# Performance work log

Hardware: AMD Instinct MI355X
Metric: run time of the kernel (lower is better)

## Reference

```python
import jax, jax.numpy as jnp
import numpy as np

B, T, D, H = 4, 2048, 1024, 16
Hd = D // H


def setup_inputs() -> dict:
    key = jax.random.key(0)
    ks = jax.random.split(key, 6)
    s = 1.0 / np.sqrt(D)
    return {
        "x": jax.random.normal(ks[0], (B, T, D), dtype=jnp.float32),
        "mask": jnp.zeros((B, T), dtype=bool),
        "Wq": jax.random.normal(ks[1], (D, D), dtype=jnp.float32) * s,
        "bq": jnp.zeros((D,), dtype=jnp.float32),
        "Wk": jax.random.normal(ks[2], (D, D), dtype=jnp.float32) * s,
        "bk": jnp.zeros((D,), dtype=jnp.float32),
        "Wv": jax.random.normal(ks[3], (D, D), dtype=jnp.float32) * s,
        "bv": jnp.zeros((D,), dtype=jnp.float32),
        "Wo": jax.random.normal(ks[4], (D, D), dtype=jnp.float32) * s,
        "bo": jnp.zeros((D,), dtype=jnp.float32),
    }


def reference(x, mask, Wq, bq, Wk, bk, Wv, bv, Wo, bo):
    b, t, d = x.shape
    # projections -> [B, T, H, Hd]
    Q = (x @ Wq + bq).reshape(b, t, H, Hd)
    K = (x @ Wk + bk).reshape(b, t, H, Hd)
    V = (x @ Wv + bv).reshape(b, t, H, Hd)
    scale = jnp.asarray(Hd, x.dtype) ** -0.5
    # full score matrix [B, H, Tq, Tk] (matches the naive torch impl)
    attn = jnp.einsum("bqhd,bkhd->bhqk", Q, K) * scale
    attn = jnp.where(mask[:, None, None, :], jnp.asarray(-1e9, attn.dtype), attn)
    attn = jax.nn.softmax(attn, axis=-1)
    out = jnp.einsum("bhqk,bkhd->bqhd", attn, V).reshape(b, t, d)
    return out @ Wo + bo
```

## Files before the change

kernel.cpp:

```cpp
#include <hip/hip_runtime.h>

using bf16 = __bf16;
typedef bf16 bf16x4 __attribute__((ext_vector_type(4)));
typedef bf16 bf16x8 __attribute__((ext_vector_type(8)));
typedef float f32x4 __attribute__((ext_vector_type(4)));
typedef float f32x8 __attribute__((ext_vector_type(8)));

#define MFMA16(a, b, c) __builtin_amdgcn_mfma_f32_16x16x32_bf16(a, b, c, 0, 0, 0)

constexpr int Bb = 4, Tt = 2048, Dd = 1024, Hh = 16, Hd = 64;
constexpr int Mrows = Bb * Tt;
constexpr float CEXP = 0.18033688011112042f;

__device__ __forceinline__ void gload_lds16(const bf16* g, bf16* lds_base) {
  __builtin_amdgcn_global_load_lds((const __attribute__((address_space(1))) void*)g,
                                   (__attribute__((address_space(3))) void*)lds_base,
                                   16, 0, 0);
}

__global__ void cast_f32_bf16_kernel(const float* __restrict__ in, bf16* __restrict__ out) {
  size_t i = ((size_t)blockIdx.x * 256 + threadIdx.x) * 8;
  f32x8 v = *(const f32x8*)(in + i);
  *(bf16x8*)(out + i) = __builtin_convertvector(v, bf16x8);
}

__global__ void transpose_cast_w4_kernel(const float* __restrict__ Wq, const float* __restrict__ Wk,
                                         const float* __restrict__ Wv, const float* __restrict__ Wo,
                                         bf16* __restrict__ Wt, bf16* __restrict__ Wot) {
  __shared__ alignas(16) float tile[64][68];
  const int tid = threadIdx.x;
  const int n0 = blockIdx.x * 64, k0 = blockIdx.y * 64, z = blockIdx.z;
  const float* W = (z == 0) ? Wq : (z == 1) ? Wk : (z == 2) ? Wv : Wo;
  bf16* dst = (z == 3) ? Wot : (Wt + (size_t)z * Dd * Dd);
  const float scale = (z == 0) ? CEXP : 1.0f;
#pragma unroll
  for (int it = 0; it < 4; ++it) {
    int chunk = tid + it * 256;
    int kr = chunk >> 4, c4 = chunk & 15;
    f32x4 v = *(const f32x4*)(W + (size_t)(k0 + kr) * Dd + n0 + c4 * 4);
    *(f32x4*)&tile[kr][c4 * 4] = v * scale;
  }
  __syncthreads();
#pragma unroll
  for (int it = 0; it < 2; ++it) {
    int chunk = tid + it * 256;
    int n = chunk & 63, k8 = chunk >> 6;
    bf16x8 o;
#pragma unroll
    for (int j = 0; j < 8; ++j) o[j] = (bf16)tile[k8 * 8 + j][n];
    *(bf16x8*)(dst + (size_t)(n0 + n) * Dd + k0 + k8 * 8) = o;
  }
}

__global__ void pack_bias_kernel(const float* __restrict__ bq, const float* __restrict__ bk,
                                 const float* __restrict__ bv, float* __restrict__ outb) {
  int i = blockIdx.x * 256 + threadIdx.x;
  float v = (i < 1024) ? bq[i] * CEXP : (i < 2048 ? bk[i - 1024] : bv[i - 2048]);
  outb[i] = v;
}

constexpr int QBM = 128, QBN = 256, QBK = 32, QNT = Dd / QBK;

#define VMW(n) asm volatile("s_waitcnt vmcnt(" #n ")" ::: "memory")

__global__ __launch_bounds__(512, 2)
void gemm_qkv_kernel(const bf16* __restrict__ A, const bf16* __restrict__ Bt,
                     const float* __restrict__ bias, bf16* __restrict__ QK,
                     bf16* __restrict__ Vt) {
  constexpr int KD = Dd;
  __shared__ alignas(16) bf16 As[3][QBM * QBK];
  __shared__ alignas(16) bf16 Bs[3][QBN * QBK];
  const int tid = threadIdx.x;
  const int lane = tid & 63, wave = tid >> 6;
  const int col = lane & 15, quad = lane >> 4;
  const int wr = wave >> 2, wc = wave & 3;
  const size_t m0 = (size_t)blockIdx.x * QBM, n0 = (size_t)blockIdx.y * QBN;

  const int u = (lane & 7) ^ (lane >> 3);
  const int srow = 2 * (lane >> 3) + (u >> 2);
  const int scol = (u & 3) * 8;
  const bf16* Abase = A + (m0 + srow) * (size_t)KD + scol;
  const bf16* Bbase = Bt + (n0 + srow) * (size_t)KD + scol;

  const int pswz = (((col & 1) << 2) | quad) ^ (col >> 1);
  const int afb = wr * 2048 + (col >> 1) * 64 + pswz * 8;
  const int bfb = wc * 2048 + (col >> 1) * 64 + pswz * 8;

  f32x4 acc[4][4];
#pragma unroll
  for (int i = 0; i < 4; ++i)
#pragma unroll
    for (int j = 0; j < 4; ++j)
#pragma unroll
      for (int r = 0; r < 4; ++r) acc[i][j][r] = 0.f;

#define QSTAGE(t, sl) do { \
    gload_lds16(Abase + (size_t)(t) * QBK + (size_t)(wave * 16) * KD, &As[sl][wave * 512]); \
    gload_lds16(Bbase + (size_t)(t) * QBK + (size_t)(2 * wave) * 16 * KD, &Bs[sl][(2 * wave) * 512]); \
    gload_lds16(Bbase + (size_t)(t) * QBK + (size_t)(2 * wave + 1) * 16 * KD, &Bs[sl][(2 * wave + 1) * 512]); \
  } while (0)

#define QKV_TILE(cur, DOSTAGE, VM) do { \
    bf16x8 af[4], bfv[4]; \
    _Pragma("unroll") for (int j = 0; j < 4; ++j) bfv[j] = *(const bf16x8*)&Bs[cur][bfb + j * 512]; \
    _Pragma("unroll") for (int i = 0; i < 4; ++i) af[i] = *(const bf16x8*)&As[cur][afb + i * 512]; \
    DOSTAGE; \
    asm volatile("s_waitcnt lgkmcnt(0)" ::: "memory"); \
    __builtin_amdgcn_s_setprio(1); \
    _Pragma("unroll") for (int i = 0; i < 4; ++i) \
      _Pragma("unroll") for (int j = 0; j < 4; ++j) acc[i][j] = MFMA16(af[i], bfv[j], acc[i][j]); \
    __builtin_amdgcn_s_setprio(0); \
    VM; \
    __builtin_amdgcn_s_barrier(); \
  } while (0)

  QSTAGE(0, 0);
  QSTAGE(1, 1);
  VMW(3);
  __builtin_amdgcn_s_barrier();

#pragma unroll 1
  for (int t = 0; t < QNT - 2; t += 3) {
    QKV_TILE(0, QSTAGE(t + 2, 2), VMW(3));
    QKV_TILE(1, QSTAGE(t + 3, 0), VMW(3));
    QKV_TILE(2, QSTAGE(t + 4, 1), VMW(3));
  }
  QKV_TILE(0, (void)0, VMW(0));
  QKV_TILE(1, (void)0, (void)0);

  if (n0 < 2048) {
#pragma unroll
    for (int i = 0; i < 4; ++i)
#pragma unroll
      for (int j = 0; j < 4; ++j) {
        size_t row = m0 + wr * 64 + i * 16 + quad * 4;
        size_t c = n0 + wc * 64 + j * 16 + col;
        float bv = bias[c];
#pragma unroll
        for (int r = 0; r < 4; ++r) QK[(row + r) * 2048 + c] = (bf16)(acc[i][j][r] + bv);
      }
  } else {
#pragma unroll
    for (int i = 0; i < 4; ++i)
#pragma unroll
      for (int j = 0; j < 4; ++j) {
        size_t row = m0 + wr * 64 + i * 16 + quad * 4;
        int c = (int)(n0 + wc * 64 + j * 16 + col);
        float bv = bias[c];
        int dall = c - 2048, hh = dall >> 6, dd = dall & 63;
        int bi = (int)(row >> 11), trow = (int)(row & 2047);
        bf16x4 pk;
#pragma unroll
        for (int r = 0; r < 4; ++r) pk[r] = (bf16)(acc[i][j][r] + bv);
        *(bf16x4*)&Vt[((size_t)(bi * Hh + hh) * Hd + dd) * Tt + trow] = pk;
      }
  }
#undef QKV_TILE
#undef QSTAGE
}

__global__ __launch_bounds__(512, 2)
void gemm_out_kernel(const bf16* __restrict__ A, const bf16* __restrict__ Bt,
                     const float* __restrict__ bias, float* __restrict__ C) {
  constexpr int KD = Dd, NN = Dd;
  __shared__ alignas(16) bf16 As[3][QBM * QBK];
  __shared__ alignas(16) bf16 Bs[3][QBN * QBK];
  const int tid = threadIdx.x;
  const int lane = tid & 63, wave = tid >> 6;
  const int col = lane & 15, quad = lane >> 4;
  const int wr = wave >> 2, wc = wave & 3;
  const size_t m0 = (size_t)blockIdx.x * QBM, n0 = (size_t)blockIdx.y * QBN;

  const int u = (lane & 7) ^ (lane >> 3);
  const int srow = 2 * (lane >> 3) + (u >> 2);
  const int scol = (u & 3) * 8;
  const bf16* Abase = A + (m0 + srow) * (size_t)KD + scol;
  const bf16* Bbase = Bt + (n0 + srow) * (size_t)KD + scol;

  const int pswz = (((col & 1) << 2) | quad) ^ (col >> 1);
  const int afb = wr * 2048 + (col >> 1) * 64 + pswz * 8;
  const int bfb = wc * 2048 + (col >> 1) * 64 + pswz * 8;

  f32x4 acc[4][4];
#pragma unroll
  for (int i = 0; i < 4; ++i)
#pragma unroll
    for (int j = 0; j < 4; ++j)
#pragma unroll
      for (int r = 0; r < 4; ++r) acc[i][j][r] = 0.f;

#define OSTAGE(t, sl) do { \
    gload_lds16(Abase + (size_t)(t) * QBK + (size_t)(wave * 16) * KD, &As[sl][wave * 512]); \
    gload_lds16(Bbase + (size_t)(t) * QBK + (size_t)(2 * wave) * 16 * KD, &Bs[sl][(2 * wave) * 512]); \
    gload_lds16(Bbase + (size_t)(t) * QBK + (size_t)(2 * wave + 1) * 16 * KD, &Bs[sl][(2 * wave + 1) * 512]); \
  } while (0)

#define OUT_TILE(cur, DOSTAGE, VM) do { \
    bf16x8 af[4], bfv[4]; \
    _Pragma("unroll") for (int j = 0; j < 4; ++j) bfv[j] = *(const bf16x8*)&Bs[cur][bfb + j * 512]; \
    _Pragma("unroll") for (int i = 0; i < 4; ++i) af[i] = *(const bf16x8*)&As[cur][afb + i * 512]; \
    DOSTAGE; \
    asm volatile("s_waitcnt lgkmcnt(0)" ::: "memory"); \
    __builtin_amdgcn_s_setprio(1); \
    _Pragma("unroll") for (int i = 0; i < 4; ++i) \
      _Pragma("unroll") for (int j = 0; j < 4; ++j) acc[i][j] = MFMA16(af[i], bfv[j], acc[i][j]); \
    __builtin_amdgcn_s_setprio(0); \
    VM; \
    __builtin_amdgcn_s_barrier(); \
  } while (0)

  OSTAGE(0, 0);
  OSTAGE(1, 1);
  VMW(3);
  __builtin_amdgcn_s_barrier();

#pragma unroll 1
  for (int t = 0; t < QNT - 2; t += 3) {
    OUT_TILE(0, OSTAGE(t + 2, 2), VMW(3));
    OUT_TILE(1, OSTAGE(t + 3, 0), VMW(3));
    OUT_TILE(2, OSTAGE(t + 4, 1), VMW(3));
  }
  OUT_TILE(0, (void)0, VMW(0));
  OUT_TILE(1, (void)0, (void)0);

#pragma unroll
  for (int i = 0; i < 4; ++i)
#pragma unroll
    for (int j = 0; j < 4; ++j) {
      size_t row = m0 + wr * 64 + i * 16 + quad * 4;
      size_t c = n0 + wc * 64 + j * 16 + col;
      float bv = bias[c];
#pragma unroll
      for (int r = 0; r < 4; ++r) C[(row + r) * (size_t)NN + c] = acc[i][j][r] + bv;
    }
#undef OUT_TILE
#undef OSTAGE
}

__global__ __launch_bounds__(256, 2)
void flash_attn_kernel(const bf16* __restrict__ qk, const bf16* __restrict__ vt,
                       const unsigned char* __restrict__ mask, bf16* __restrict__ ao) {
  __shared__ alignas(16) bf16 Ks[3][64 * 64];
  __shared__ alignas(16) bf16 Vs[3][64 * 64];

  const int tid = threadIdx.x;
  const int wave = tid >> 6, lane = tid & 63;
  const int col = lane & 15, quad = lane >> 4;
  const int id = blockIdx.x;
  const int hb = id & 63, qi = id >> 6;
  const int h = hb & 15, b = hb >> 4;
  const int qbase0 = qi * 128 + wave * 32;

  const bf16* Qp = qk + (size_t)(b * Tt) * 2048 + h * Hd;
  const bf16* Kp = Qp + 1024;
  const bf16* Vp = vt + ((size_t)(b * Hh + h) * Hd) * Tt;
  const unsigned char* mp = mask + b * Tt;

  unsigned long long anym;
  {
    const unsigned long long* mq = (const unsigned long long*)mp;
    unsigned long long acc = 0;
#pragma unroll
    for (int j = 0; j < 4; ++j) acc |= mq[lane * 4 + j];
    anym = __ballot(acc != 0ull);
  }

  bf16x8 qf[2][2];
#pragma unroll
  for (int t = 0; t < 2; ++t)
#pragma unroll
    for (int kk = 0; kk < 2; ++kk)
      qf[t][kk] = *(const bf16x8*)(Qp + (size_t)(qbase0 + t * 16 + col) * 2048 + kk * 32 + quad * 8);

  const int u = (lane & 7) ^ (lane >> 3);
  const int g0 = 2 * wave, g1 = 2 * wave + 1;
  const bf16* Ksrc0 = Kp + (size_t)(g0 * 8 + (lane >> 3)) * 2048 + u * 8;
  const bf16* Ksrc1 = Kp + (size_t)(g1 * 8 + (lane >> 3)) * 2048 + u * 8;
  const bf16* Vsrc0 = Vp + (size_t)(g0 * 8 + (lane >> 3)) * 2048 + u * 8;
  const bf16* Vsrc1 = Vp + (size_t)(g1 * 8 + (lane >> 3)) * 2048 + u * 8;

#define FSTAGE(t, sl) do { \
    gload_lds16(Ksrc0 + (size_t)(t) * 64 * 2048, &Ks[sl][g0 * 512]); \
    gload_lds16(Ksrc1 + (size_t)(t) * 64 * 2048, &Ks[sl][g1 * 512]); \
    gload_lds16(Vsrc0 + (t) * 64, &Vs[sl][g0 * 512]); \
    gload_lds16(Vsrc1 + (t) * 64, &Vs[sl][g1 * 512]); \
  } while (0)

  f32x4 oacc[2][4];
  f32x4 lones[2];
#pragma unroll
  for (int t = 0; t < 2; ++t) {
#pragma unroll
    for (int r = 0; r < 4; ++r) lones[t][r] = 0.f;
#pragma unroll
    for (int n = 0; n < 4; ++n)
#pragma unroll
      for (int r = 0; r < 4; ++r) oacc[t][n][r] = 0.f;
  }
  const f32x4 zero4 = {0.f, 0.f, 0.f, 0.f};
  bf16x8 onev;
#pragma unroll
  for (int j = 0; j < 8; ++j) onev[j] = (bf16)1.0f;

  const int fslot0 = ((0 * 4 + quad) ^ (col & 7)) * 8;
  const int fslot1 = ((1 * 4 + quad) ^ (col & 7)) * 8;
  const int voff = (quad & 1) * 4;

#define FITER(cur, II, DOSTAGE, VM) do { \
    const int kb = (II) * 64; \
    DOSTAGE; \
    bf16x8 kf[4][2], vfs[4][2]; \
    _Pragma("unroll") for (int kt = 0; kt < 4; ++kt) { \
      kf[kt][0] = *(const bf16x8*)&Ks[cur][(kt * 16 + col) * 64 + fslot0]; \
      kf[kt][1] = *(const bf16x8*)&Ks[cur][(kt * 16 + col) * 64 + fslot1]; \
    } \
    _Pragma("unroll") for (int n = 0; n < 4; ++n) { \
      const int row = (n * 16 + col) * 64; \
      const int rx = col & 7; \
      _Pragma("unroll") for (int kk = 0; kk < 2; ++kk) { \
        bf16x4 lo = *(const bf16x4*)&Vs[cur][row + ((kk * 4 + 0 + (quad >> 1)) ^ rx) * 8 + voff]; \
        bf16x4 hi = *(const bf16x4*)&Vs[cur][row + ((kk * 4 + 2 + (quad >> 1)) ^ rx) * 8 + voff]; \
        vfs[n][kk] = __builtin_shufflevector(lo, hi, 0, 1, 2, 3, 4, 5, 6, 7); \
      } \
    } \
    _Pragma("unroll") for (int t = 0; t < 2; ++t) { \
      f32x4 s[4]; \
      _Pragma("unroll") for (int kt = 0; kt < 4; ++kt) s[kt] = MFMA16(kf[kt][0], qf[t][0], zero4); \
      _Pragma("unroll") for (int kt = 0; kt < 4; ++kt) s[kt] = MFMA16(kf[kt][1], qf[t][1], s[kt]); \
      if ((anym >> (2 * (II))) & 3ull) { \
        _Pragma("unroll") for (int kt = 0; kt < 4; ++kt) \
          _Pragma("unroll") for (int r = 0; r < 4; ++r) \
            if (mp[kb + kt * 16 + quad * 4 + r] != 0) s[kt][r] = -1e9f; \
      } \
      f32x4 e[4]; \
      _Pragma("unroll") for (int kt = 0; kt < 4; ++kt) \
        _Pragma("unroll") for (int r = 0; r < 4; ++r) e[kt][r] = __builtin_amdgcn_exp2f(s[kt][r]); \
      bf16x4 c0 = __builtin_convertvector(e[0], bf16x4); \
      bf16x4 c1 = __builtin_convertvector(e[1], bf16x4); \
      bf16x4 c2 = __builtin_convertvector(e[2], bf16x4); \
      bf16x4 c3 = __builtin_convertvector(e[3], bf16x4); \
      bf16x8 pf0 = __builtin_shufflevector(c0, c1, 0, 1, 2, 3, 4, 5, 6, 7); \
      bf16x8 pf1 = __builtin_shufflevector(c2, c3, 0, 1, 2, 3, 4, 5, 6, 7); \
      _Pragma("unroll") for (int n = 0; n < 4; ++n) { \
        oacc[t][n] = MFMA16(pf0, vfs[n][0], oacc[t][n]); \
        oacc[t][n] = MFMA16(pf1, vfs[n][1], oacc[t][n]); \
      } \
      lones[t] = MFMA16(pf0, onev, lones[t]); \
      lones[t] = MFMA16(pf1, onev, lones[t]); \
    } \
    VM; \
    __builtin_amdgcn_s_barrier(); \
  } while (0)

  FSTAGE(0, 0);
  FSTAGE(1, 1);
  VMW(4);
  __builtin_amdgcn_s_barrier();

#pragma unroll 1
  for (int ii = 0; ii < 30; ii += 3) {
    FITER(0, ii + 0, FSTAGE(ii + 2, 2), VMW(4));
    FITER(1, ii + 1, FSTAGE(ii + 3, 0), VMW(4));
    FITER(2, ii + 2, FSTAGE(ii + 4, 1), VMW(4));
  }
  FITER(0, 30, (void)0, VMW(0));
  FITER(1, 31, (void)0, (void)0);

#undef FITER
#undef FSTAGE

#pragma unroll
  for (int t = 0; t < 2; ++t) {
    f32x4 rl;
#pragma unroll
    for (int r = 0; r < 4; ++r) rl[r] = __builtin_amdgcn_rcpf(lones[t][r]);
#pragma unroll
    for (int n = 0; n < 4; ++n)
#pragma unroll
      for (int r = 0; r < 4; ++r) {
        size_t q = (size_t)b * Tt + qbase0 + t * 16 + quad * 4 + r;
        ao[q * Dd + h * Hd + n * 16 + col] = (bf16)(oacc[t][n][r] * rl[r]);
      }
  }
}

extern "C" void kernel_launch(void* const* d_in, const int* in_sizes, int n_in,
                              void* d_out, int out_size, void* d_ws, size_t ws_size,
                              hipStream_t stream) {
  const float* x = (const float*)d_in[0];
  const unsigned char* mask = (const unsigned char*)d_in[1];
  const float* Wq = (const float*)d_in[2];
  const float* bq = (const float*)d_in[3];
  const float* Wk = (const float*)d_in[4];
  const float* bk = (const float*)d_in[5];
  const float* Wv = (const float*)d_in[6];
  const float* bv = (const float*)d_in[7];
  const float* Wo = (const float*)d_in[8];
  const float* bo = (const float*)d_in[9];
  float* out = (float*)d_out;

  char* ws = (char*)d_ws;
  size_t off = 0;
  auto alloc = [&](size_t bytes) {
    char* p = ws + off;
    off += (bytes + 255) & ~(size_t)255;
    return p;
  };
  bf16* xb  = (bf16*)alloc((size_t)Mrows * Dd * 2);
  bf16* Wt  = (bf16*)alloc((size_t)3 * Dd * Dd * 2);
  bf16* Wot = (bf16*)alloc((size_t)Dd * Dd * 2);
  bf16* QK  = (bf16*)alloc((size_t)Mrows * 2048 * 2);
  bf16* Vt  = (bf16*)alloc((size_t)Bb * Hh * Hd * Tt * 2);
  float* bqkv = (float*)alloc((size_t)3 * Dd * 4);

  cast_f32_bf16_kernel<<<Mrows * Dd / (256 * 8), 256, 0, stream>>>(x, xb);
  transpose_cast_w4_kernel<<<dim3(16, 16, 4), 256, 0, stream>>>(Wq, Wk, Wv, Wo, Wt, Wot);
  pack_bias_kernel<<<12, 256, 0, stream>>>(bq, bk, bv, bqkv);

  gemm_qkv_kernel<<<dim3(Mrows / QBM, 3 * Dd / QBN), 512, 0, stream>>>(
      xb, Wt, bqkv, QK, Vt);

  bf16* AO = xb;
  flash_attn_kernel<<<dim3(1024), 256, 0, stream>>>(QK, Vt, mask, AO);
  gemm_out_kernel<<<dim3(Mrows / QBM, Dd / QBN), 512, 0, stream>>>(
      AO, Wot, bo, out);
}
```

Measured before the change: 281.0 us.

## Double query rows per wave in flash attention to reuse K/V fragments

Each wave now handles 64 query rows (four 16-row tiles) instead of 32, and each block covers 256 queries, so the grid drops from 1024 to 512 blocks. K and V fragments read from LDS are reused across four query tiles, which halves the LDS traffic and K/V global staging per query. The cost is higher register pressure from larger accumulators and the score array, possibly lower occupancy under launch_bounds(256,2), and fewer blocks to spread across the CUs.

```diff
diff --git a/kernel.cpp b/kernel.cpp
--- a/kernel.cpp
+++ b/kernel.cpp
@@ -249,7 +249,7 @@
   const int id = blockIdx.x;
   const int hb = id & 63, qi = id >> 6;
   const int h = hb & 15, b = hb >> 4;
-  const int qbase0 = qi * 128 + wave * 32;
+  const int qbase0 = qi * 256 + wave * 64;
 
   const bf16* Qp = qk + (size_t)(b * Tt) * 2048 + h * Hd;
   const bf16* Kp = Qp + 1024;
@@ -265,9 +265,9 @@
     anym = __ballot(acc != 0ull);
   }
 
-  bf16x8 qf[2][2];
-#pragma unroll
-  for (int t = 0; t < 2; ++t)
+  bf16x8 qf[4][2];
+#pragma unroll
+  for (int t = 0; t < 4; ++t)
 #pragma unroll
     for (int kk = 0; kk < 2; ++kk)
       qf[t][kk] = *(const bf16x8*)(Qp + (size_t)(qbase0 + t * 16 + col) * 2048 + kk * 32 + quad * 8);
@@ -286,10 +286,10 @@
     gload_lds16(Vsrc1 + (t) * 64, &Vs[sl][g1 * 512]); \
   } while (0)
 
-  f32x4 oacc[2][4];
-  f32x4 lones[2];
-#pragma unroll
-  for (int t = 0; t < 2; ++t) {
+  f32x4 oacc[4][4];
+  f32x4 lones[4];
+#pragma unroll
+  for (int t = 0; t < 4; ++t) {
 #pragma unroll
     for (int r = 0; r < 4; ++r) lones[t][r] = 0.f;
 #pragma unroll
@@ -309,44 +309,56 @@
 #define FITER(cur, II, DOSTAGE, VM) do { \
     const int kb = (II) * 64; \
     DOSTAGE; \
-    bf16x8 kf[4][2], vfs[4][2]; \
+    f32x4 s[4][4]; \
     _Pragma("unroll") for (int kt = 0; kt < 4; ++kt) { \
-      kf[kt][0] = *(const bf16x8*)&Ks[cur][(kt * 16 + col) * 64 + fslot0]; \
-      kf[kt][1] = *(const bf16x8*)&Ks[cur][(kt * 16 + col) * 64 + fslot1]; \
+      bf16x8 kf0 = *(const bf16x8*)&Ks[cur][(kt * 16 + col) * 64 + fslot0]; \
+      bf16x8 kf1 = *(const bf16x8*)&Ks[cur][(kt * 16 + col) * 64 + fslot1]; \
+      _Pragma("unroll") for (int t = 0; t < 4; ++t) { \
+        s[t][kt] = MFMA16(kf0, qf[t][0], zero4); \
+        s[t][kt] = MFMA16(kf1, qf[t][1], s[t][kt]); \
+      } \
+    } \
+    if ((anym >> (2 * (II))) & 3ull) { \
+      _Pragma("unroll") for (int kt = 0; kt < 4; ++kt) \
+        _Pragma("unroll") for (int r = 0; r < 4; ++r) \
+          if (mp[kb + kt * 16 + quad * 4 + r] != 0) { \
+            _Pragma("unroll") for (int t = 0; t < 4; ++t) s[t][kt][r] = -1e9f; \
+          } \
+    } \
+    bf16x8 pf[4][2]; \
+    _Pragma("unroll") for (int t = 0; t < 4; ++t) { \
+      f32x4 e0, e1, e2, e3; \
+      _Pragma("unroll") for (int r = 0; r < 4; ++r) { \
+        e0[r] = __builtin_amdgcn_exp2f(s[t][0][r]); \
+        e1[r] = __builtin_amdgcn_exp2f(s[t][1][r]); \
+        e2[r] = __builtin_amdgcn_exp2f(s[t][2][r]); \
+        e3[r] = __builtin_amdgcn_exp2f(s[t][3][r]); \
+      } \
+      bf16x4 c0 = __builtin_convertvector(e0, bf16x4); \
+      bf16x4 c1 = __builtin_convertvector(e1, bf16x4); \
+      bf16x4 c2 = __builtin_convertvector(e2, bf16x4); \
+      bf16x4 c3 = __builtin_convertvector(e3, bf16x4); \
+      pf[t][0] = __builtin_shufflevector(c0, c1, 0, 1, 2, 3, 4, 5, 6, 7); \
+      pf[t][1] = __builtin_shufflevector(c2, c3, 0, 1, 2, 3, 4, 5, 6, 7); \
     } \
     _Pragma("unroll") for (int n = 0; n < 4; ++n) { \
       const int row = (n * 16 + col) * 64; \
       const int rx = col & 7; \
-      _Pragma("unroll") for (int kk = 0; kk < 2; ++kk) { \
-        bf16x4 lo = *(const bf16x4*)&Vs[cur][row + ((kk * 4 + 0 + (quad >> 1)) ^ rx) * 8 + voff]; \
-        bf16x4 hi = *(const bf16x4*)&Vs[cur][row + ((kk * 4 + 2 + (quad >> 1)) ^ rx) * 8 + voff]; \
-        vfs[n][kk] = __builtin_shufflevector(lo, hi, 0, 1, 2, 3, 4, 5, 6, 7); \
+      bf16x8 v0, v1; \
+      { bf16x4 lo = *(const bf16x4*)&Vs[cur][row + ((0 + (quad >> 1)) ^ rx) * 8 + voff]; \
+        bf16x4 hi = *(const bf16x4*)&Vs[cur][row + ((2 + (quad >> 1)) ^ rx) * 8 + voff]; \
+        v0 = __builtin_shufflevector(lo, hi, 0, 1, 2, 3, 4, 5, 6, 7); } \
+      { bf16x4 lo = *(const bf16x4*)&Vs[cur][row + ((4 + (quad >> 1)) ^ rx) * 8 + voff]; \
+        bf16x4 hi = *(const bf16x4*)&Vs[cur][row + ((6 + (quad >> 1)) ^ rx) * 8 + voff]; \
+        v1 = __builtin_shufflevector(lo, hi, 0, 1, 2, 3, 4, 5, 6, 7); } \
+      _Pragma("unroll") for (int t = 0; t < 4; ++t) { \
+        oacc[t][n] = MFMA16(pf[t][0], v0, oacc[t][n]); \
+        oacc[t][n] = MFMA16(pf[t][1], v1, oacc[t][n]); \
       } \
     } \
-    _Pragma("unroll") for (int t = 0; t < 2; ++t) { \
-      f32x4 s[4]; \
-      _Pragma("unroll") for (int kt = 0; kt < 4; ++kt) s[kt] = MFMA16(kf[kt][0], qf[t][0], zero4); \
-      _Pragma("unroll") for (int kt = 0; kt < 4; ++kt) s[kt] = MFMA16(kf[kt][1], qf[t][1], s[kt]); \
-      if ((anym >> (2 * (II))) & 3ull) { \
-        _Pragma("unroll") for (int kt = 0; kt < 4; ++kt) \
-          _Pragma("unroll") for (int r = 0; r < 4; ++r) \
-            if (mp[kb + kt * 16 + quad * 4 + r] != 0) s[kt][r] = -1e9f; \
-      } \
-      f32x4 e[4]; \
-      _Pragma("unroll") for (int kt = 0; kt < 4; ++kt) \
-        _Pragma("unroll") for (int r = 0; r < 4; ++r) e[kt][r] = __builtin_amdgcn_exp2f(s[kt][r]); \
-      bf16x4 c0 = __builtin_convertvector(e[0], bf16x4); \
-      bf16x4 c1 = __builtin_convertvector(e[1], bf16x4); \
-      bf16x4 c2 = __builtin_convertvector(e[2], bf16x4); \
-      bf16x4 c3 = __builtin_convertvector(e[3], bf16x4); \
-      bf16x8 pf0 = __builtin_shufflevector(c0, c1, 0, 1, 2, 3, 4, 5, 6, 7); \
-      bf16x8 pf1 = __builtin_shufflevector(c2, c3, 0, 1, 2, 3, 4, 5, 6, 7); \
-      _Pragma("unroll") for (int n = 0; n < 4; ++n) { \
-        oacc[t][n] = MFMA16(pf0, vfs[n][0], oacc[t][n]); \
-        oacc[t][n] = MFMA16(pf1, vfs[n][1], oacc[t][n]); \
-      } \
-      lones[t] = MFMA16(pf0, onev, lones[t]); \
-      lones[t] = MFMA16(pf1, onev, lones[t]); \
+    _Pragma("unroll") for (int t = 0; t < 4; ++t) { \
+      lones[t] = MFMA16(pf[t][0], onev, lones[t]); \
+      lones[t] = MFMA16(pf[t][1], onev, lones[t]); \
     } \
     VM; \
     __builtin_amdgcn_s_barrier(); \
@@ -370,7 +382,7 @@
 #undef FSTAGE
 
 #pragma unroll
-  for (int t = 0; t < 2; ++t) {
+  for (int t = 0; t < 4; ++t) {
     f32x4 rl;
 #pragma unroll
     for (int r = 0; r < 4; ++r) rl[r] = __builtin_amdgcn_rcpf(lones[t][r]);
@@ -421,7 +433,7 @@
       xb, Wt, bqkv, QK, Vt);
 
   bf16* AO = xb;
-  flash_attn_kernel<<<dim3(1024), 256, 0, stream>>>(QK, Vt, mask, AO);
+  flash_attn_kernel<<<dim3(512), 256, 0, stream>>>(QK, Vt, mask, AO);
   gemm_out_kernel<<<dim3(Mrows / QBM, Dd / QBN), 512, 0, stream>>>(
       AO, Wot, bo, out);
 }
```

After: 265.3 us. -5.6%, faster.
